# Kernel tuning notes

Measured on AMD Instinct MI355X. Metric: run time of the kernel, lower is better.

## Reference

```python
import jax, jax.numpy as jnp
import numpy as np

B, CIN, OUT = 16, 64, 64
CH = CIN // 2          # depthwise group count (32)
H, W = 256, 256        # mas resolution; cen is at (H//2, W//2)

# The 8 fixed 3x3 dilation-3 kernels are center-minus-shifted-neighbor ops.
# Cross-correlation offsets (dy, dx) of the -1 tap, dilation 3:
OFFSETS = [(-3, -3), (-3, 0), (-3, 3), (0, 3), (3, 3), (3, 0), (3, -3), (0, -3)]


def setup_inputs() -> dict:
    key = jax.random.key(0)
    ks = jax.random.split(key, 9)
    cen = jax.random.normal(ks[0], (B, CIN, H // 2, W // 2), jnp.float32)
    mas = jax.random.normal(ks[1], (B, CH, H, W), jnp.float32)
    # inp_layer: Conv2d(CH, CH, k=3, s=2, p=1) + SiLU
    w_inp = jax.random.normal(ks[2], (CH, CH, 3, 3), jnp.float32) * 0.05
    b_inp = jax.random.normal(ks[3], (CH,), jnp.float32) * 0.05
    # layer1/2/3: grouped 1x1, groups=CH, per-group 8 in -> 2 out; store as [CH, 2, 8]
    w1 = jax.random.normal(ks[4], (CH, 2, 8), jnp.float32) * 0.1
    w2 = jax.random.normal(ks[5], (CH, 2, 8), jnp.float32) * 0.1
    w3 = jax.random.normal(ks[6], (CH, 2, 8), jnp.float32) * 0.1
    # out_conv: 1x1 conv, 3*CIN -> OUT, with bias
    w_out = jax.random.normal(ks[7], (OUT, 3 * CIN), jnp.float32) * 0.05
    b_out = jax.random.normal(ks[8], (OUT,), jnp.float32) * 0.05
    return {"cen": cen, "mas": mas, "w_inp": w_inp, "b_inp": b_inp,
            "w1": w1, "w2": w2, "w3": w3, "w_out": w_out, "b_out": b_out}


def _forward(cen, mas, w_inp, b_inp, w1, w2, w3, w_out, b_out):
    # stem: 3x3 stride-2 conv + SiLU  -> [B, CH, H//2, W//2]
    x = jax.lax.conv_general_dilated(
        mas, w_inp, window_strides=(2, 2), padding=((1, 1), (1, 1)),
        dimension_numbers=("NCHW", "OIHW", "NCHW"))
    x = jax.nn.silu(x + b_inp[None, :, None, None])
    b, c, h, w = x.shape
    # 8 dilated depthwise diff-convs == center minus zero-padded shifted copy
    xp = jnp.pad(x, ((0, 0), (0, 0), (3, 3), (3, 3)))
    deltas = jnp.stack(
        [x - jax.lax.dynamic_slice(xp, (0, 0, 3 + dy, 3 + dx), (b, c, h, w))
         for dy, dx in OFFSETS], axis=2)                     # [B, CH, 8, h, w]
    # grouped 1x1 gating convs (groups=CH): per-group [2,8] matmul
    g1 = jnp.einsum("bcdhw,cod->bcohw", deltas, w1)
    g2 = jnp.einsum("bcdhw,cod->bcohw", deltas, w2)
    square = (g1 * g2).reshape(b, 2 * c, h, w)               # layer1 * layer2
    dout = jnp.einsum("bcdhw,cod->bcohw", deltas, w3).reshape(b, 2 * c, h, w)
    # concat [square, dout, cen] along channels -> 1x1 out_conv
    outs = jnp.concatenate([square, dout, cen], axis=1)      # [B, 3*CIN, h, w]
    return jnp.einsum("bchw,oc->bohw", outs, w_out) + b_out[None, :, None, None]


def reference(cen, mas, w_inp, b_inp, w1, w2, w3, w_out, b_out):
    return _forward(cen, mas, w_inp, b_inp, w1, w2, w3, w_out, b_out)
```

## Files before the change

### kernel.cpp

```cpp
#include <hip/hip_runtime.h>
#include <hip/hip_bf16.h>

#define BATCH 16
#define CH    32
#define CIN   64
#define OUTC  64
#define HH    128
#define WW    128
#define HW    (HH * WW)
#define MHW   65536

typedef __attribute__((ext_vector_type(8))) short bf16x8;
typedef __attribute__((ext_vector_type(4))) float f32x4;

__device__ inline unsigned short bf16u(float x) {
  union { __hip_bfloat16 h; unsigned short s; } u;
  u.h = __float2bfloat16(x);
  return u.s;
}
__device__ inline unsigned int pack2(float lo, float hi) {
  return (unsigned int)bf16u(lo) | ((unsigned int)bf16u(hi) << 16);
}
__device__ inline float losf(unsigned u) { return __uint_as_float(u << 16); }
__device__ inline float hisf(unsigned u) { return __uint_as_float(u & 0xffff0000u); }

__global__ __launch_bounds__(256) void k_prep_weights(
    const float* __restrict__ w_out, const float* __restrict__ w_inp,
    const float* __restrict__ w3,
    unsigned short* __restrict__ wfrag, unsigned short* __restrict__ wfrag2,
    unsigned short* __restrict__ wfrag3) {
  int t = blockIdx.x * 256 + threadIdx.x;
  if (t < 9 * 2 * 64 * 8) {
    int e    = t & 7;
    int lane = (t >> 3) & 63;
    int ct   = (t >> 9) & 1;
    int tap  = t >> 10;
    int co = ct * 16 + (lane & 15);
    int ci = (lane >> 4) * 8 + e;
    wfrag[t] = bf16u(w_inp[(co * CH + ci) * 9 + tap]);
  }
  int t2 = t - 9216;
  if (t2 >= 0 && t2 < 8192) {
    int e    = t2 & 7;
    int lane = (t2 >> 3) & 63;
    int ot   = (t2 >> 9) & 3;
    int kt   = t2 >> 11;
    int o = ot * 16 + (lane & 15);
    int k = kt * 32 + (lane >> 4) * 8 + e;
    int col = (k < 64) ? k : 64 + k;
    wfrag2[t2] = bf16u(w_out[o * 192 + col]);
  }
  int t3 = t - 17408;
  if (t3 >= 0 && t3 < 18432) {
    int e    = t3 & 7;
    int lane = (t3 >> 3) & 63;
    int ot   = (t3 >> 9) & 3;
    int tap  = t3 >> 11;
    int o = ot * 16 + (lane & 15);
    int C = (lane >> 4) * 8 + e;
    const int kmap[9] = {0, 1, 2, 7, -1, 3, 6, 5, 4};
    float v = 0.f;
    if (tap == 4) {
      for (int k = 0; k < 8; ++k)
        for (int op = 0; op < 2; ++op)
          v += w_out[o * 192 + 64 + 2 * C + op] * w3[C * 16 + op * 8 + k];
    } else {
      int k = kmap[tap];
      for (int op = 0; op < 2; ++op)
        v -= w_out[o * 192 + 64 + 2 * C + op] * w3[C * 16 + op * 8 + k];
    }
    wfrag3[t3] = bf16u(v);
  }
}

#define BEE 0
#define BEO 165
#define BOE 330
#define BOO 462
#define SPITCH 36

__global__ __launch_bounds__(256, 3) void k_stem(
    const float* __restrict__ mas, const unsigned short* __restrict__ wfrag,
    const float* __restrict__ b_inp, unsigned short* __restrict__ xbuf) {
  __shared__ alignas(16) unsigned short xs[594 * SPITCH];

  const int W = blockIdx.x + 4 * blockIdx.y + 128 * blockIdx.z;
  const int F = (W & 7) * 256 + (W >> 3);
  const int bx = F & 3;
  const int by = (F >> 2) & 31;
  const int b  = F >> 7;

  const int t  = threadIdx.x;
  const int lane = t & 63;
  const int w = t >> 6;
  const int ct = w >> 1, chh = w & 1;

  const int I0 = by * 4, J0 = bx * 32;
  const int R0 = 2 * I0 - 1, C0 = 2 * J0 - 1;

  bf16x8 af[9];
#pragma unroll
  for (int tap = 0; tap < 9; ++tap)
    af[tap] = ((const bf16x8*)wfrag)[(tap * 2 + ct) * 64 + lane];

  if (t < 144) {
    int chunk = t / 9, rr = t % 9;
    int cc0 = 1 + 4 * chunk;
    int ir = R0 + rr;
    bool vrow = (ir >= 0);
    const float* gp = mas + (size_t)b * CH * MHW +
                      (size_t)(vrow ? ir : 0) * 256 + (C0 + cc0);
    int off[4];
#pragma unroll
    for (int j = 0; j < 4; ++j) {
      int cc = cc0 + j;
      int r2 = rr >> 1;
      int pix;
      if (!(rr & 1))
        pix = (cc & 1) ? BEO + r2 * 33 + ((cc - 1) >> 1)
                       : BEE + r2 * 33 + (cc >> 1);
      else
        pix = (cc & 1) ? BOO + r2 * 33 + ((cc - 1) >> 1)
                       : BOE + r2 * 33 + (cc >> 1);
      off[j] = pix * SPITCH;
    }
#pragma unroll 4
    for (int q = 0; q < 16; ++q) {
      float4 v0 = make_float4(0.f, 0.f, 0.f, 0.f);
      float4 v1 = v0;
      if (vrow) {
        v0 = *(const float4*)(gp + (size_t)(2 * q) * MHW);
        v1 = *(const float4*)(gp + (size_t)(2 * q + 1) * MHW);
      }
      *(unsigned*)&xs[off[0] + 2 * q] = pack2(v0.x, v1.x);
      *(unsigned*)&xs[off[1] + 2 * q] = pack2(v0.y, v1.y);
      *(unsigned*)&xs[off[2] + 2 * q] = pack2(v0.z, v1.z);
      *(unsigned*)&xs[off[3] + 2 * q] = pack2(v0.w, v1.w);
    }
  } else if (t < 153) {
    int rr = t - 144;
    int ir = R0 + rr;
    bool ok = (ir >= 0) && (bx > 0);
    int r2 = rr >> 1;
    int pix = (rr & 1) ? (BOE + r2 * 33) : (BEE + r2 * 33);
    const float* gp = mas + (size_t)b * CH * MHW +
                      (size_t)(ir >= 0 ? ir : 0) * 256 + (C0 >= 0 ? C0 : 0);
    int off0 = pix * SPITCH;
#pragma unroll 4
    for (int q = 0; q < 16; ++q) {
      float a0 = 0.f, a1 = 0.f;
      if (ok) {
        a0 = gp[(size_t)(2 * q) * MHW];
        a1 = gp[(size_t)(2 * q + 1) * MHW];
      }
      *(unsigned*)&xs[off0 + 2 * q] = pack2(a0, a1);
    }
  }
  __syncthreads();

  f32x4 acc[4];
#pragma unroll
  for (int il = 0; il < 4; ++il) acc[il] = 0.f;

  const int jt = chh * 16 + (lane & 15);
  const int gsh = (lane >> 4) * 8;

#pragma unroll
  for (int ky = 0; ky < 3; ++ky) {
#pragma unroll
    for (int kx = 0; kx < 3; ++kx) {
      const int tap = ky * 3 + kx;
#pragma unroll
      for (int il = 0; il < 4; ++il) {
        int pix;
        if (ky == 1) {
          pix = (kx == 1) ? (BOO + il * 33 + jt)
                          : (BOE + il * 33 + jt + (kx == 2));
        } else {
          int r2 = il + (ky >> 1);
          pix = (kx == 1) ? (BEO + r2 * 33 + jt)
                          : (BEE + r2 * 33 + jt + (kx == 2));
        }
        bf16x8 bfr = *(const bf16x8*)(xs + pix * SPITCH + gsh);
        acc[il] = __builtin_amdgcn_mfma_f32_16x16x32_bf16(
            af[tap], bfr, acc[il], 0, 0, 0);
      }
    }
  }

  float4 bia = *(const float4*)(b_inp + ct * 16 + (lane >> 4) * 4);
  const int co0 = ct * 16 + (lane >> 4) * 4;
  const int colg = J0 + jt;
#pragma unroll
  for (int il = 0; il < 4; ++il) {
    int i = I0 + il;
    float y0 = acc[il][0] + bia.x;
    float y1 = acc[il][1] + bia.y;
    float y2 = acc[il][2] + bia.z;
    float y3 = acc[il][3] + bia.w;
    float s0 = y0 / (1.f + __expf(-y0));
    float s1 = y1 / (1.f + __expf(-y1));
    float s2 = y2 / (1.f + __expf(-y2));
    float s3 = y3 / (1.f + __expf(-y3));
    uint2 uv;
    uv.x = pack2(s0, s1);
    uv.y = pack2(s2, s3);
    *(uint2*)(xbuf + ((size_t)(b * HH + i) * WW + colg) * 32 + co0) = uv;
  }
}

#define PPITCH 132

__global__ __launch_bounds__(256, 4) void k_fused(
    const unsigned short* __restrict__ xbuf, const float* __restrict__ cen,
    const float* __restrict__ w1, const float* __restrict__ w2,
    const unsigned short* __restrict__ wfrag2,
    const unsigned short* __restrict__ wfrag3,
    const float* __restrict__ b_out, float* __restrict__ out) {
  __shared__ alignas(16) unsigned short xs[196 * 36];
  __shared__ alignas(16) unsigned short panel[64][PPITCH];

  const int W = blockIdx.x + 16 * blockIdx.y + 256 * blockIdx.z;
  const int F = (W & 7) * 512 + (W >> 3);
  const int bx = F & 15;
  const int by = (F >> 4) & 15;
  const int b  = F >> 8;

  const int t  = threadIdx.x;
  const int lane = t & 63;
  const int w = t >> 6;
  const int I0 = by * 8, J0 = bx * 8;

  bf16x8 af3[9], af2[4];
#pragma unroll
  for (int tap = 0; tap < 9; ++tap)
    af3[tap] = ((const bf16x8*)wfrag3)[(tap * 4 + w) * 64 + lane];
#pragma unroll
  for (int kt = 0; kt < 4; ++kt)
    af2[kt] = ((const bf16x8*)wfrag2)[(kt * 4 + w) * 64 + lane];

#pragma unroll
  for (int j = 0; j < 8; ++j) {
    int idx = j * 256 + t;
    int cc = idx >> 6, p = idx & 63;
    int py = p >> 3, px = p & 7;
    const float* cp = cen + ((size_t)(b * CIN + 2 * cc) * HH + I0 + py) * WW
                      + J0 + px;
    *(unsigned int*)&panel[p][64 + 2 * cc] = pack2(cp[0], cp[HW]);
  }

  {
    int row = t >> 4, col = t & 15;
    if (row < 14 && col < 14) {
      int gi = I0 - 3 + row, gj = J0 - 3 + col;
      bool ok = (gi >= 0 && gi < HH && gj >= 0 && gj < WW);
      const unsigned short* gp = xbuf +
          ((size_t)((size_t)b * HH + (ok ? gi : 0)) * WW + (ok ? gj : 0)) * 32;
      unsigned short* sp = xs + (row * 14 + col) * 36;
#pragma unroll
      for (int s = 0; s < 4; ++s) {
        uint4 v = make_uint4(0u, 0u, 0u, 0u);
        if (ok) v = *(const uint4*)(gp + 8 * s);
        *(uint2*)(sp + 8 * s)     = make_uint2(v.x, v.y);
        *(uint2*)(sp + 8 * s + 4) = make_uint2(v.z, v.w);
      }
    }
  }
  __syncthreads();

  f32x4 acc[4];
#pragma unroll
  for (int pt = 0; pt < 4; ++pt) acc[pt] = 0.f;

  const int prow = lane & 15;
  const int gsh = (lane >> 4) * 8;
#pragma unroll
  for (int pt = 0; pt < 4; ++pt) {
    int p = pt * 16 + prow;
    int ppy = p >> 3, ppx = p & 7;
#pragma unroll
    for (int ty = 0; ty < 3; ++ty)
#pragma unroll
      for (int tx = 0; tx < 3; ++tx) {
        int pos = (ppy + 3 * ty) * 14 + ppx + 3 * tx;
        bf16x8 bfr = *(const bf16x8*)(xs + pos * 36 + gsh);
        acc[pt] = __builtin_amdgcn_mfma_f32_16x16x32_bf16(
            af3[ty * 3 + tx], bfr, acc[pt], 0, 0, 0);
      }
  }

  {
    const int py = lane >> 3, px = lane & 7;
    const int posc = (py + 3) * 14 + (px + 3);
    int pos8[8];
    pos8[0] = (py + 0) * 14 + px + 0;
    pos8[1] = (py + 0) * 14 + px + 3;
    pos8[2] = (py + 0) * 14 + px + 6;
    pos8[3] = (py + 3) * 14 + px + 6;
    pos8[4] = (py + 6) * 14 + px + 6;
    pos8[5] = (py + 6) * 14 + px + 3;
    pos8[6] = (py + 6) * 14 + px + 0;
    pos8[7] = (py + 3) * 14 + px + 0;

#pragma unroll
    for (int j = 0; j < 4; ++j) {
      int c2 = __builtin_amdgcn_readfirstlane(j * 4 + w);
      const float* w1lo = w1 + (2 * c2) * 16;
      const float* w1hi = w1 + (2 * c2 + 1) * 16;
      const float* w2lo = w2 + (2 * c2) * 16;
      const float* w2hi = w2 + (2 * c2 + 1) * 16;
      unsigned uc = *(const unsigned*)(xs + posc * 36 + 2 * c2);
      float clo = losf(uc), chi = hisf(uc);
      float g1l0 = 0, g1l1 = 0, g2l0 = 0, g2l1 = 0;
      float g1h0 = 0, g1h1 = 0, g2h0 = 0, g2h1 = 0;
#pragma unroll
      for (int k = 0; k < 8; ++k) {
        unsigned us = *(const unsigned*)(xs + pos8[k] * 36 + 2 * c2);
        float dlo = clo - losf(us);
        float dhi = chi - hisf(us);
        g1l0 += dlo * w1lo[k];  g1l1 += dlo * w1lo[8 + k];
        g2l0 += dlo * w2lo[k];  g2l1 += dlo * w2lo[8 + k];
        g1h0 += dhi * w1hi[k];  g1h1 += dhi * w1hi[8 + k];
        g2h0 += dhi * w2hi[k];  g2h1 += dhi * w2hi[8 + k];
      }
      uint2 wv;
      wv.x = pack2(g1l0 * g2l0, g1l1 * g2l1);
      wv.y = pack2(g1h0 * g2h0, g1h1 * g2h1);
      *(uint2*)&panel[lane][4 * c2] = wv;
    }
  }
  __syncthreads();

#pragma unroll
  for (int pt = 0; pt < 4; ++pt) {
#pragma unroll
    for (int kt = 0; kt < 4; ++kt) {
      bf16x8 bfr = *(const bf16x8*)(&panel[pt * 16 + prow][kt * 32 + gsh]);
      acc[pt] = __builtin_amdgcn_mfma_f32_16x16x32_bf16(
          af2[kt], bfr, acc[pt], 0, 0, 0);
    }
  }

  float4 bo = *(const float4*)(b_out + w * 16 + (lane >> 4) * 4);
#pragma unroll
  for (int pt = 0; pt < 4; ++pt) {
    int p = pt * 16 + prow;
    int ppy = p >> 3, ppx = p & 7;
#pragma unroll
    for (int r = 0; r < 4; ++r) {
      int o = w * 16 + (lane >> 4) * 4 + r;
      out[((b * OUTC + o) * HH + I0 + ppy) * WW + J0 + ppx] =
          acc[pt][r] + ((const float*)&bo)[r];
    }
  }
}

extern "C" void kernel_launch(void* const* d_in, const int* in_sizes, int n_in,
                              void* d_out, int out_size, void* d_ws, size_t ws_size,
                              hipStream_t stream) {
  const float* cen   = (const float*)d_in[0];
  const float* mas   = (const float*)d_in[1];
  const float* w_inp = (const float*)d_in[2];
  const float* b_inp = (const float*)d_in[3];
  const float* w1    = (const float*)d_in[4];
  const float* w2    = (const float*)d_in[5];
  const float* w3    = (const float*)d_in[6];
  const float* w_out = (const float*)d_in[7];
  const float* b_out = (const float*)d_in[8];
  float* out = (float*)d_out;

  unsigned short* xbuf   = (unsigned short*)d_ws;
  unsigned short* wfrag  = xbuf + (size_t)BATCH * HW * 32;
  unsigned short* wfrag2 = wfrag + 9216;
  unsigned short* wfrag3 = wfrag2 + 8192;

  hipLaunchKernelGGL(k_prep_weights, dim3(140), dim3(256), 0, stream,
                     w_out, w_inp, w3, wfrag, wfrag2, wfrag3);
  hipLaunchKernelGGL(k_stem, dim3(4, 32, 16), dim3(256), 0, stream,
                     mas, wfrag, b_inp, xbuf);
  hipLaunchKernelGGL(k_fused, dim3(16, 16, 16), dim3(256), 0, stream,
                     xbuf, cen, w1, w2, wfrag2, wfrag3, b_out, out);
}
```

Measured before the change: 115.2 us.

## Pre-convert mas to NHWC bf16 in a separate pass before the stem conv

Adds a k_prep_mas kernel that transposes the fp32 NCHW input into a channels-last bf16 buffer. The stem can then fill its shared-memory tile with 16-byte vector loads and a simple row-major index, replacing the strided per-channel fp32 gathers and the even/odd phase layout. The cost is an extra full read of mas plus a 64 MB write and reread through the workspace, and one more kernel launch.

```diff
diff --git a/kernel.cpp b/kernel.cpp
--- a/kernel.cpp
+++ b/kernel.cpp
@@ -73,16 +73,43 @@
   }
 }
 
-#define BEE 0
-#define BEO 165
-#define BOE 330
-#define BOO 462
+__global__ __launch_bounds__(256) void k_prep_mas(
+    const float* __restrict__ mas, unsigned short* __restrict__ masb) {
+  __shared__ alignas(16) unsigned short tile[256 * 36];
+
+  const int W = blockIdx.x + 256 * blockIdx.y;
+  const int F = (W & 7) * 512 + (W >> 3);
+  const int r = F & 255;
+  const int b = F >> 8;
+  const int t = threadIdx.x;
+
+  const float* gp = mas + (size_t)b * CH * MHW + (size_t)r * 256 + t;
+#pragma unroll 8
+  for (int q = 0; q < 16; ++q) {
+    float v0 = gp[(size_t)(2 * q) * MHW];
+    float v1 = gp[(size_t)(2 * q + 1) * MHW];
+    *(unsigned*)&tile[t * 36 + 2 * q] = pack2(v0, v1);
+  }
+  __syncthreads();
+
+  unsigned short* op = masb + (((size_t)b * 256 + r) * 256) * 32;
+#pragma unroll
+  for (int it = 0; it < 4; ++it) {
+    int idx = it * 256 + t;
+    int px = idx >> 2, seg = idx & 3;
+    uint2 a  = *(const uint2*)&tile[px * 36 + seg * 8];
+    uint2 bq = *(const uint2*)&tile[px * 36 + seg * 8 + 4];
+    *(uint4*)(op + (size_t)px * 32 + seg * 8) = make_uint4(a.x, a.y, bq.x, bq.y);
+  }
+}
+
 #define SPITCH 36
 
 __global__ __launch_bounds__(256, 3) void k_stem(
-    const float* __restrict__ mas, const unsigned short* __restrict__ wfrag,
+    const unsigned short* __restrict__ masb,
+    const unsigned short* __restrict__ wfrag,
     const float* __restrict__ b_inp, unsigned short* __restrict__ xbuf) {
-  __shared__ alignas(16) unsigned short xs[594 * SPITCH];
+  __shared__ alignas(16) unsigned short xs[585 * SPITCH];
 
   const int W = blockIdx.x + 4 * blockIdx.y + 128 * blockIdx.z;
   const int F = (W & 7) * 256 + (W >> 3);
@@ -103,58 +130,17 @@
   for (int tap = 0; tap < 9; ++tap)
     af[tap] = ((const bf16x8*)wfrag)[(tap * 2 + ct) * 64 + lane];
 
-  if (t < 144) {
-    int chunk = t / 9, rr = t % 9;
-    int cc0 = 1 + 4 * chunk;
-    int ir = R0 + rr;
-    bool vrow = (ir >= 0);
-    const float* gp = mas + (size_t)b * CH * MHW +
-                      (size_t)(vrow ? ir : 0) * 256 + (C0 + cc0);
-    int off[4];
-#pragma unroll
-    for (int j = 0; j < 4; ++j) {
-      int cc = cc0 + j;
-      int r2 = rr >> 1;
-      int pix;
-      if (!(rr & 1))
-        pix = (cc & 1) ? BEO + r2 * 33 + ((cc - 1) >> 1)
-                       : BEE + r2 * 33 + (cc >> 1);
-      else
-        pix = (cc & 1) ? BOO + r2 * 33 + ((cc - 1) >> 1)
-                       : BOE + r2 * 33 + (cc >> 1);
-      off[j] = pix * SPITCH;
-    }
-#pragma unroll 4
-    for (int q = 0; q < 16; ++q) {
-      float4 v0 = make_float4(0.f, 0.f, 0.f, 0.f);
-      float4 v1 = v0;
-      if (vrow) {
-        v0 = *(const float4*)(gp + (size_t)(2 * q) * MHW);
-        v1 = *(const float4*)(gp + (size_t)(2 * q + 1) * MHW);
-      }
-      *(unsigned*)&xs[off[0] + 2 * q] = pack2(v0.x, v1.x);
-      *(unsigned*)&xs[off[1] + 2 * q] = pack2(v0.y, v1.y);
-      *(unsigned*)&xs[off[2] + 2 * q] = pack2(v0.z, v1.z);
-      *(unsigned*)&xs[off[3] + 2 * q] = pack2(v0.w, v1.w);
-    }
-  } else if (t < 153) {
-    int rr = t - 144;
-    int ir = R0 + rr;
-    bool ok = (ir >= 0) && (bx > 0);
-    int r2 = rr >> 1;
-    int pix = (rr & 1) ? (BOE + r2 * 33) : (BEE + r2 * 33);
-    const float* gp = mas + (size_t)b * CH * MHW +
-                      (size_t)(ir >= 0 ? ir : 0) * 256 + (C0 >= 0 ? C0 : 0);
-    int off0 = pix * SPITCH;
-#pragma unroll 4
-    for (int q = 0; q < 16; ++q) {
-      float a0 = 0.f, a1 = 0.f;
-      if (ok) {
-        a0 = gp[(size_t)(2 * q) * MHW];
-        a1 = gp[(size_t)(2 * q + 1) * MHW];
-      }
-      *(unsigned*)&xs[off0 + 2 * q] = pack2(a0, a1);
-    }
+  const unsigned short* mb = masb + (size_t)b * 256 * 256 * 32;
+  for (int idx = t; idx < 585 * 4; idx += 256) {
+    int px = idx >> 2, seg = idx & 3;
+    int rr = px / 65, cc = px - rr * 65;
+    int gr = R0 + rr, gc = C0 + cc;
+    uint4 v = make_uint4(0u, 0u, 0u, 0u);
+    if (gr >= 0 && gc >= 0)
+      v = *(const uint4*)(mb + ((size_t)gr * 256 + gc) * 32 + seg * 8);
+    unsigned short* sp = xs + px * SPITCH + seg * 8;
+    *(uint2*)(sp)     = make_uint2(v.x, v.y);
+    *(uint2*)(sp + 4) = make_uint2(v.z, v.w);
   }
   __syncthreads();
 
@@ -172,15 +158,7 @@
       const int tap = ky * 3 + kx;
 #pragma unroll
       for (int il = 0; il < 4; ++il) {
-        int pix;
-        if (ky == 1) {
-          pix = (kx == 1) ? (BOO + il * 33 + jt)
-                          : (BOE + il * 33 + jt + (kx == 2));
-        } else {
-          int r2 = il + (ky >> 1);
-          pix = (kx == 1) ? (BEO + r2 * 33 + jt)
-                          : (BEE + r2 * 33 + jt + (kx == 2));
-        }
+        int pix = (2 * il + ky) * 65 + 2 * jt + kx;
         bf16x8 bfr = *(const bf16x8*)(xs + pix * SPITCH + gsh);
         acc[il] = __builtin_amdgcn_mfma_f32_16x16x32_bf16(
             af[tap], bfr, acc[il], 0, 0, 0);
@@ -369,15 +347,18 @@
   const float* b_out = (const float*)d_in[8];
   float* out = (float*)d_out;
 
-  unsigned short* xbuf   = (unsigned short*)d_ws;
+  unsigned short* masb   = (unsigned short*)d_ws;
+  unsigned short* xbuf   = masb + (size_t)BATCH * 256 * 256 * 32;
   unsigned short* wfrag  = xbuf + (size_t)BATCH * HW * 32;
   unsigned short* wfrag2 = wfrag + 9216;
   unsigned short* wfrag3 = wfrag2 + 8192;
 
+  hipLaunchKernelGGL(k_prep_mas, dim3(256, 16), dim3(256), 0, stream,
+                     mas, masb);
   hipLaunchKernelGGL(k_prep_weights, dim3(140), dim3(256), 0, stream,
                      w_out, w_inp, w3, wfrag, wfrag2, wfrag3);
   hipLaunchKernelGGL(k_stem, dim3(4, 32, 16), dim3(256), 0, stream,
-                     mas, wfrag, b_inp, xbuf);
+                     masb, wfrag, b_inp, xbuf);
   hipLaunchKernelGGL(k_fused, dim3(16, 16, 16), dim3(256), 0, stream,
                      xbuf, cen, w1, w2, wfrag2, wfrag3, b_out, out);
 }
```

Result: no change. 117.0 us (+1.5%).
